# Optimization experiments

Measured on AMD Instinct MI355X. Metric: run time of the kernel, lower is better.

## Reference

```python
import jax, jax.numpy as jnp
import numpy as np
from jax import lax

SOBEL_X = jnp.array([[-1., 0., 1.], [-2., 0., 2.], [-1., 0., 1.]], jnp.float32)
SCHARR_X = jnp.array([[-3., 0., 3.], [-10., 0., 10.], [-3., 0., 3.]], jnp.float32)

# year routing map baked in (configure()): 2019->sobel(0), 2020->scharr(1), default learnable(2)

def _dwconv(x, k2d):
    """Depthwise 3x3 conv with the same 2D kernel per channel, padding=1."""
    C = x.shape[1]
    kern = jnp.broadcast_to(k2d, (C, 1, 3, 3))
    return lax.conv_general_dilated(
        x, kern, window_strides=(1, 1), padding='SAME',
        dimension_numbers=('NCHW', 'OIHW', 'NCHW'), feature_group_count=C)


def _edge_mag(x, kx, ky, eps):
    gx = _dwconv(x, kx)
    gy = _dwconv(x, ky)
    return jnp.sqrt(gx * gx + gy * gy + eps)


def setup_inputs() -> dict:
    key = jax.random.key(0)
    k1, k2 = jax.random.split(key)
    x = jax.random.normal(k1, (32, 9, 256, 256), jnp.float32)
    year = 2018 + jax.random.randint(k2, (32,), 0, 4)  # years 2018..2021
    alpha = jnp.asarray(0.5, jnp.float32)
    scale = jnp.ones((1,), jnp.float32) * 0.1
    return {"x": x, "alpha": alpha, "scale": scale, "year": year}


def reference(x, alpha, scale, year):
    B = x.shape[0]
    # fixed operators
    sobel_out = _edge_mag(x, SOBEL_X, SOBEL_X.T, 1e-8)
    scharr_out = _edge_mag(x, SCHARR_X, SCHARR_X.T, 1e-8)
    # learnable operator: sigmoid-mixed kernel, normalized by max abs
    a = jax.nn.sigmoid(alpha)
    kx = a * SOBEL_X + (1.0 - a) * SCHARR_X
    kx = kx / jnp.max(jnp.abs(kx))
    ky = kx.T  # sobel_y = sobel_x.T and scharr_y = scharr_x.T, mix commutes with transpose
    learnable_out = _edge_mag(x, kx, ky, 1e-6) * jax.nn.sigmoid(scale)
    # per-sample routing: 2019 -> sobel, 2020 -> scharr, else default learnable
    op_idx = jnp.where(year == 2019, 0, jnp.where(year == 2020, 1, 2))
    stacked = jnp.stack([sobel_out, scharr_out, learnable_out])  # [3,B,C,H,W]
    mixed = stacked[op_idx, jnp.arange(B)]
    return mixed
```

## Files before the change

kernel.cpp:

```cpp
#include <hip/hip_runtime.h>
#include <math.h>

#define BATCH 32
#define CHANS 9
#define HH 256
#define WW 256

typedef float f32x4 __attribute__((ext_vector_type(4)));

__global__ __launch_bounds__(256) void edge_router_kernel(
    const float* __restrict__ x,
    const float* __restrict__ alpha_p,
    const float* __restrict__ scale_p,
    const int*   __restrict__ year,
    float* __restrict__ out)
{
    const int tid   = threadIdx.x;
    const int lane  = tid & 63;
    const int gwave = blockIdx.x * 4 + (tid >> 6);
    const int pair  = gwave & 127;
    const int plane = gwave >> 7;
    const int b     = plane / CHANS;
    const int r0    = pair * 2;
    const int r1    = r0 + 1;
    const int xq    = lane * 4;

    const float* __restrict__ p = x   + (size_t)plane * (HH * WW);
    float*       __restrict__ q = out + (size_t)plane * (HH * WW);

    const int ym = r0 > 0 ? r0 - 1 : 0;
    const int yp = r1 < HH - 1 ? r1 + 1 : HH - 1;
    f32x4 va = *reinterpret_cast<const f32x4*>(p + (size_t)ym * WW + xq);
    f32x4 vb = *reinterpret_cast<const f32x4*>(p + (size_t)r0 * WW + xq);
    f32x4 vc = *reinterpret_cast<const f32x4*>(p + (size_t)r1 * WW + xq);
    f32x4 vd = *reinterpret_cast<const f32x4*>(p + (size_t)yp * WW + xq);
    if (r0 == 0)      va = (f32x4)0.f;
    if (r1 == HH - 1) vd = (f32x4)0.f;

    const int yr = year[b];
    float w0, w1, eps, post;
    if (yr == 2019) {
        w0 = 1.f; w1 = 2.f; eps = 1e-8f; post = 1.f;
    } else if (yr == 2020) {
        w0 = 3.f; w1 = 10.f; eps = 1e-8f; post = 1.f;
    } else {
        const float a = 1.f / (1.f + expf(-alpha_p[0]));
        const float m = 10.f - 8.f * a;
        w0 = (3.f - 2.f * a) / m;
        w1 = 1.f;
        eps = 1e-6f;
        post = 1.f / (1.f + expf(-scale_p[0]));
    }

    auto finish_row = [&](f32x4 t, f32x4 u, int y) {
        float tl = __shfl_up(t.w, 1);
        float ul = __shfl_up(u.w, 1);
        if (lane == 0)  { tl = 0.f; ul = 0.f; }
        float tr = __shfl_down(t.x, 1);
        float ur = __shfl_down(u.x, 1);
        if (lane == 63) { tr = 0.f; ur = 0.f; }

        f32x4 gx, gy;
        gx.x = t.y - tl;   gx.y = t.z - t.x;
        gx.z = t.w - t.y;  gx.w = tr - t.z;
        gy.x = fmaf(w1, u.x, w0 * (ul + u.y));
        gy.y = fmaf(w1, u.y, w0 * (u.x + u.z));
        gy.z = fmaf(w1, u.z, w0 * (u.y + u.w));
        gy.w = fmaf(w1, u.w, w0 * (u.z + ur));

        f32x4 o;
        o.x = sqrtf(fmaf(gx.x, gx.x, fmaf(gy.x, gy.x, eps))) * post;
        o.y = sqrtf(fmaf(gx.y, gx.y, fmaf(gy.y, gy.y, eps))) * post;
        o.z = sqrtf(fmaf(gx.z, gx.z, fmaf(gy.z, gy.z, eps))) * post;
        o.w = sqrtf(fmaf(gx.w, gx.w, fmaf(gy.w, gy.w, eps))) * post;

        *reinterpret_cast<f32x4*>(q + (size_t)y * WW + xq) = o;
    };

    f32x4 t0, u0, t1, u1;
    t0.x = fmaf(w1, vb.x, w0 * (va.x + vc.x));
    t0.y = fmaf(w1, vb.y, w0 * (va.y + vc.y));
    t0.z = fmaf(w1, vb.z, w0 * (va.z + vc.z));
    t0.w = fmaf(w1, vb.w, w0 * (va.w + vc.w));
    u0 = vc - va;
    t1.x = fmaf(w1, vc.x, w0 * (vb.x + vd.x));
    t1.y = fmaf(w1, vc.y, w0 * (vb.y + vd.y));
    t1.z = fmaf(w1, vc.z, w0 * (vb.z + vd.z));
    t1.w = fmaf(w1, vc.w, w0 * (vb.w + vd.w));
    u1 = vd - vb;

    finish_row(t0, u0, r0);
    finish_row(t1, u1, r1);
}

extern "C" void kernel_launch(void* const* d_in, const int* in_sizes, int n_in,
                              void* d_out, int out_size, void* d_ws, size_t ws_size,
                              hipStream_t stream) {
    const float* x     = (const float*)d_in[0];
    const float* alpha = (const float*)d_in[1];
    const float* scale = (const float*)d_in[2];
    const int*   year  = (const int*)  d_in[3];
    float* out = (float*)d_out;

    const int pairs  = BATCH * CHANS * (HH / 2);
    const int blocks = pairs / 4;
    edge_router_kernel<<<blocks, 256, 0, stream>>>(x, alpha, scale, year, out);
}
```

Baseline: 132.7 us.

## Stage 10-row halo strip in LDS via direct global-to-LDS loads

Each block now covers an 8-row strip of a plane and loads the 10 rows it needs (strip plus halo) into shared memory once, using the global_load_lds builtin. The four waves then read their overlapping 4-row windows from LDS. Previously every wave fetched its own 4 rows from global memory. This cuts redundant halo reads from 2x to 1.25x, at the cost of a block barrier and an LDS round trip.

```diff
diff --git a/kernel.cpp b/kernel.cpp
--- a/kernel.cpp
+++ b/kernel.cpp
@@ -7,6 +7,8 @@
 #define WW 256
 
 typedef float f32x4 __attribute__((ext_vector_type(4)));
+typedef const __attribute__((address_space(1))) void* gas_ptr;
+typedef __attribute__((address_space(3))) void* las_ptr;
 
 __global__ __launch_bounds__(256) void edge_router_kernel(
     const float* __restrict__ x,
@@ -15,27 +17,30 @@
     const int*   __restrict__ year,
     float* __restrict__ out)
 {
-    const int tid   = threadIdx.x;
-    const int lane  = tid & 63;
-    const int gwave = blockIdx.x * 4 + (tid >> 6);
-    const int pair  = gwave & 127;
-    const int plane = gwave >> 7;
+    __shared__ float lds[10][WW];
+
+    const int tid  = threadIdx.x;
+    const int lane = tid & 63;
+    const int w    = tid >> 6;
+
+    const int strip = blockIdx.x & 31;
+    const int plane = blockIdx.x >> 5;
     const int b     = plane / CHANS;
-    const int r0    = pair * 2;
-    const int r1    = r0 + 1;
+    const int r0    = strip * 8;
     const int xq    = lane * 4;
 
     const float* __restrict__ p = x   + (size_t)plane * (HH * WW);
-    float*       __restrict__ q = out + (size_t)plane * (HH * WW);
+    float*       __restrict__ q = out + (size_t)plane * (HH * WW) + xq;
 
-    const int ym = r0 > 0 ? r0 - 1 : 0;
-    const int yp = r1 < HH - 1 ? r1 + 1 : HH - 1;
-    f32x4 va = *reinterpret_cast<const f32x4*>(p + (size_t)ym * WW + xq);
-    f32x4 vb = *reinterpret_cast<const f32x4*>(p + (size_t)r0 * WW + xq);
-    f32x4 vc = *reinterpret_cast<const f32x4*>(p + (size_t)r1 * WW + xq);
-    f32x4 vd = *reinterpret_cast<const f32x4*>(p + (size_t)yp * WW + xq);
-    if (r0 == 0)      va = (f32x4)0.f;
-    if (r1 == HH - 1) vd = (f32x4)0.f;
+    auto load_row = [&](int l) {
+        int y = r0 - 1 + l;
+        y = y < 0 ? 0 : (y > HH - 1 ? HH - 1 : y);
+        const float* g = p + (size_t)y * WW + xq;
+        __builtin_amdgcn_global_load_lds((gas_ptr)g, (las_ptr)&lds[l][0], 16, 0, 0);
+    };
+    load_row(w);
+    load_row(w + 4);
+    if (w < 2) load_row(w + 8);
 
     const int yr = year[b];
     float w0, w1, eps, post;
@@ -51,6 +56,17 @@
         eps = 1e-6f;
         post = 1.f / (1.f + expf(-scale_p[0]));
     }
+
+    __syncthreads();
+
+    const int R0 = r0 + 2 * w;
+    const int R1 = R0 + 1;
+    f32x4 va = *reinterpret_cast<const f32x4*>(&lds[2 * w + 0][xq]);
+    f32x4 vb = *reinterpret_cast<const f32x4*>(&lds[2 * w + 1][xq]);
+    f32x4 vc = *reinterpret_cast<const f32x4*>(&lds[2 * w + 2][xq]);
+    f32x4 vd = *reinterpret_cast<const f32x4*>(&lds[2 * w + 3][xq]);
+    if (R0 == 0)      va = (f32x4)0.f;
+    if (R1 == HH - 1) vd = (f32x4)0.f;
 
     auto finish_row = [&](f32x4 t, f32x4 u, int y) {
         float tl = __shfl_up(t.w, 1);
@@ -74,7 +90,7 @@
         o.z = sqrtf(fmaf(gx.z, gx.z, fmaf(gy.z, gy.z, eps))) * post;
         o.w = sqrtf(fmaf(gx.w, gx.w, fmaf(gy.w, gy.w, eps))) * post;
 
-        *reinterpret_cast<f32x4*>(q + (size_t)y * WW + xq) = o;
+        *reinterpret_cast<f32x4*>(q + (size_t)y * WW) = o;
     };
 
     f32x4 t0, u0, t1, u1;
@@ -89,8 +105,8 @@
     t1.w = fmaf(w1, vc.w, w0 * (vb.w + vd.w));
     u1 = vd - vb;
 
-    finish_row(t0, u0, r0);
-    finish_row(t1, u1, r1);
+    finish_row(t0, u0, R0);
+    finish_row(t1, u1, R1);
 }
 
 extern "C" void kernel_launch(void* const* d_in, const int* in_sizes, int n_in,
@@ -102,7 +118,6 @@
     const int*   year  = (const int*)  d_in[3];
     float* out = (float*)d_out;
 
-    const int pairs  = BATCH * CHANS * (HH / 2);
-    const int blocks = pairs / 4;
+    const int blocks = BATCH * CHANS * (HH / 8);
     edge_router_kernel<<<blocks, 256, 0, stream>>>(x, alpha, scale, year, out);
 }
```

Measured after the change: 132.8 us. About the same (+0.1%).
